# Optimization experiments

Measured on AMD Instinct MI355X. Metric: run time of the kernel, lower is better.

Reference implementation:

```python
import jax, jax.numpy as jnp
import numpy as np

B, T, C = 2, 2048, 1024
H = 16
D = C // H  # head size 64


def setup_inputs() -> dict:
    key = jax.random.key(0)
    ks = jax.random.split(key, 9)
    s = 0.02
    return {
        "x": jax.random.normal(ks[0], (B, T, C), dtype=jnp.float32),
        "Wq": jax.random.normal(ks[1], (C, C), dtype=jnp.float32) * s,
        "bq": jnp.zeros((C,), dtype=jnp.float32),
        "Wk": jax.random.normal(ks[2], (C, C), dtype=jnp.float32) * s,
        "bk": jnp.zeros((C,), dtype=jnp.float32),
        "Wv": jax.random.normal(ks[3], (C, C), dtype=jnp.float32) * s,
        "bv": jnp.zeros((C,), dtype=jnp.float32),
        "Wo": jax.random.normal(ks[4], (C, C), dtype=jnp.float32) * s,
        "bo": jnp.zeros((C,), dtype=jnp.float32),
    }


def reference(x, Wq, bq, Wk, bk, Wv, bv, Wo, bo):
    b, t, c = x.shape
    scale = 1.0 / jnp.sqrt(jnp.asarray(D, dtype=x.dtype))
    # projections (torch Linear: x @ W.T + b), then split heads -> [B,H,T,D]
    def split_heads(y):
        return y.reshape(b, t, H, D).transpose(0, 2, 1, 3)
    q = split_heads(x @ Wq.T + bq)
    k = split_heads(x @ Wk.T + bk)
    v = split_heads(x @ Wv.T + bv)
    # scores [B,H,T,T], causal mask (triu above diagonal = -inf)
    attn = jnp.einsum("bhqd,bhkd->bhqk", q, k) * scale
    causal = jnp.tril(jnp.ones((t, t), dtype=bool))  # True = keep
    attn = jnp.where(causal[None, None], attn, -jnp.inf)
    attn = jax.nn.softmax(attn, axis=-1)
    # dropout p=0.0 -> identity
    y = jnp.einsum("bhqk,bhkd->bhqd", attn, v)
    y = y.transpose(0, 2, 1, 3).reshape(b, t, c)
    return y @ Wo.T + bo
```

## Files before the change

kernel.cpp:

```cpp
#include <hip/hip_runtime.h>
#include <hip/hip_bf16.h>
#include <stdint.h>
#include <stddef.h>


typedef __bf16 bf16;
typedef __attribute__((ext_vector_type(8))) __bf16 bf16x8;
typedef __attribute__((ext_vector_type(4))) __bf16 bf16x4;
typedef __attribute__((ext_vector_type(4))) float floatx4;

#define MFMA_16x16x32(A, B, C) __builtin_amdgcn_mfma_f32_16x16x32_bf16(A, B, C, 0, 0, 0)

static constexpr int T_SEQ = 2048;
static constexpr int CDIM  = 1024;

__device__ __forceinline__ void gl2lds16(const bf16* g, bf16* l) {
  __builtin_amdgcn_global_load_lds(
      (const __attribute__((address_space(1))) uint32_t*)g,
      (__attribute__((address_space(3))) uint32_t*)l, 16, 0, 0);
}

__global__ __launch_bounds__(256) void convert_kernel(
    const float* __restrict__ x, const float* __restrict__ Wq,
    const float* __restrict__ Wk, const float* __restrict__ Wv,
    const float* __restrict__ Wo,
    bf16* __restrict__ Xb, bf16* __restrict__ Wqkvb, bf16* __restrict__ Wob) {
  size_t i = ((size_t)blockIdx.x * 256 + threadIdx.x) * 4;
  const float* src;
  bf16* dst;
  size_t off;
  if (i < 4194304) {
    src = x; dst = Xb; off = i;
  } else {
    size_t r = i - 4194304;
    int wsel = (int)(r >> 20);
    off = r & 1048575;
    src = (wsel == 0) ? Wq : (wsel == 1) ? Wk : (wsel == 2) ? Wv : Wo;
    dst = (wsel < 3) ? (Wqkvb + ((size_t)wsel << 20)) : Wob;
  }
  float4 v = *(const float4*)(src + off);
  bf16x4 o;
  o[0] = (bf16)v.x; o[1] = (bf16)v.y; o[2] = (bf16)v.z; o[3] = (bf16)v.w;
  *(bf16x4*)(dst + off) = o;
}

__global__ __launch_bounds__(256) void gemm_qkv(
    const bf16* __restrict__ Xb, const bf16* __restrict__ Wqkvb,
    const float* __restrict__ bq, const float* __restrict__ bk,
    const float* __restrict__ bv,
    bf16* __restrict__ Qb, bf16* __restrict__ Kb, bf16* __restrict__ Vtb) {
  __shared__ __align__(16) bf16 smem[12288];
  bf16* As = smem;
  bf16* Bs = smem + 4096;
  bf16* Cs = smem;

  const int bM = blockIdx.x & 63;
  const int bN = blockIdx.x >> 6;
  const int tid = threadIdx.x;
  const int w = tid >> 6, l = tid & 63;
  const int wm = w & 1, wn = w >> 1;
  const int lr = l >> 3, cl = l & 7;
  const int fr = l & 15, q4 = l >> 4;
  const int fc = fr;

  floatx4 acc[2][4];
#pragma unroll
  for (int mi = 0; mi < 2; ++mi)
#pragma unroll
    for (int ni = 0; ni < 4; ++ni)
#pragma unroll
      for (int r = 0; r < 4; ++r) acc[mi][ni][r] = 0.0f;

  for (int k0 = 0; k0 < CDIM; k0 += 64) {
#pragma unroll
    for (int i = 0; i < 2; ++i) {
      int row = i * 32 + w * 8 + lr;
      int cg = cl ^ (row & 7);
      gl2lds16(Xb + (size_t)(bM * 64 + row) * CDIM + k0 + cg * 8,
               As + row * 64 + cl * 8);
    }
#pragma unroll
    for (int i = 0; i < 4; ++i) {
      int row = i * 32 + w * 8 + lr;
      int cg = cl ^ (row & 7);
      gl2lds16(Wqkvb + (size_t)(bN * 128 + row) * CDIM + k0 + cg * 8,
               Bs + row * 64 + cl * 8);
    }
    __syncthreads();
#pragma unroll
    for (int kk = 0; kk < 2; ++kk) {
      const int cgk = kk * 4 + q4;
      bf16x8 af[2], bfr[4];
#pragma unroll
      for (int mi = 0; mi < 2; ++mi) {
        int row = wm * 32 + mi * 16 + fr;
        af[mi] = *(const bf16x8*)(As + row * 64 + (cgk ^ (row & 7)) * 8);
      }
#pragma unroll
      for (int ni = 0; ni < 4; ++ni) {
        int row = wn * 64 + ni * 16 + fr;
        bfr[ni] = *(const bf16x8*)(Bs + row * 64 + (cgk ^ (row & 7)) * 8);
      }
#pragma unroll
      for (int mi = 0; mi < 2; ++mi)
#pragma unroll
        for (int ni = 0; ni < 4; ++ni)
          acc[mi][ni] = MFMA_16x16x32(af[mi], bfr[ni], acc[mi][ni]);
    }
    __syncthreads();
  }

  const int seg = bN >> 3;
  const float QSCALE = 0.125f * 1.44269504089f;
  const float* bp = (seg == 0) ? bq : (seg == 1) ? bk : bv;

#pragma unroll
  for (int ni = 0; ni < 4; ++ni) {
    int jl = wn * 64 + ni * 16 + fc;
    float bias = bp[(bN * 128 + jl) & 1023];
#pragma unroll
    for (int mi = 0; mi < 2; ++mi)
#pragma unroll
      for (int r = 0; r < 4; ++r) {
        int ttl = wm * 32 + mi * 16 + q4 * 4 + r;
        float val = acc[mi][ni][r] + bias;
        if (seg == 0) val *= QSCALE;
        int addr = (seg == 2) ? jl * 72 + ttl : ttl * 136 + jl;
        Cs[addr] = (bf16)val;
      }
  }
  __syncthreads();

  if (seg < 2) {
    bf16* basep = (seg == 0) ? Qb : Kb;
    const int chunk = tid & 15;
    const int rb = (tid >> 4) * 4;
#pragma unroll
    for (int u = 0; u < 4; ++u) {
      int maj = rb + u;
      bf16x8 vdat = *(const bf16x8*)(Cs + maj * 136 + chunk * 8);
      int n = bM * 64 + maj;
      int b = n >> 11, tt = n & 2047;
      int j = bN * 128 + chunk * 8;
      int h = (j >> 6) & 15, d = j & 63;
      *(bf16x8*)(basep + (((size_t)(b * 16 + h) * T_SEQ + tt) << 6) + d) = vdat;
    }
  } else {
    const int chunk = tid & 7;
    const int rb = (tid >> 3) * 4;
#pragma unroll
    for (int u = 0; u < 4; ++u) {
      int maj = rb + u;
      bf16x8 vdat = *(const bf16x8*)(Cs + maj * 72 + chunk * 8);
      int j = bN * 128 + maj;
      int h = (j >> 6) & 15, d = j & 63;
      int n0 = bM * 64 + chunk * 8;
      int b = n0 >> 11, tt0 = n0 & 2047;
      *(bf16x8*)(Vtb + ((size_t)(b * 16 + h) * 64 + d) * T_SEQ + tt0) = vdat;
    }
  }
}

__global__ __launch_bounds__(256, 4) void flash_attn(
    const bf16* __restrict__ Qb, const bf16* __restrict__ Kb,
    const bf16* __restrict__ Vtb, bf16* __restrict__ Ao) {
  __shared__ __align__(16) bf16 Ks[64 * 64];
  __shared__ __align__(16) bf16 Ps[4][16 * 72];

  const int bh = blockIdx.x;
  const int ymap = blockIdx.y;
  const int a = ymap & 7, kq = ymap >> 3;
  const int qt = (kq == 0) ? 31 - a : (kq == 1) ? 16 + a : (kq == 2) ? 15 - a : a;
  const int b = bh >> 4, h = bh & 15;
  const int tid = threadIdx.x;
  const int w = tid >> 6, l = tid & 63;
  const int fc = l & 15, q4 = l >> 4;
  const int lr = l >> 3, cl = l & 7;

  const bf16* Qg = Qb + (size_t)bh * T_SEQ * 64;
  const bf16* Kg = Kb + (size_t)bh * T_SEQ * 64;
  const bf16* Vg = Vtb + (size_t)bh * 64 * T_SEQ;

  const int qrow = qt * 64 + w * 16 + fc;
  bf16x8 qf[2];
  qf[0] = *(const bf16x8*)(Qg + (size_t)qrow * 64 + q4 * 8);
  qf[1] = *(const bf16x8*)(Qg + (size_t)qrow * 64 + 32 + q4 * 8);

  const bf16* Vl = Vg + (size_t)fc * T_SEQ + q4 * 8;

  bf16x8 ones;
#pragma unroll
  for (int i = 0; i < 8; ++i) ones[i] = (bf16)1.0f;

  floatx4 o[4];
  floatx4 lacc;
#pragma unroll
  for (int ds = 0; ds < 4; ++ds)
#pragma unroll
    for (int r = 0; r < 4; ++r) o[ds][r] = 0.0f;
#pragma unroll
  for (int r = 0; r < 4; ++r) lacc[r] = 0.0f;

  for (int kv = 0; kv <= qt; ++kv) {
    const size_t kvb = (size_t)kv * 64;
#pragma unroll
    for (int i = 0; i < 2; ++i) {
      int row = i * 32 + w * 8 + lr;
      int cg = cl ^ (row & 7);
      gl2lds16(Kg + (kvb + row) * 64 + cg * 8, Ks + row * 64 + cl * 8);
    }
    __syncthreads();

    bf16x8 vf[2][4];
#pragma unroll
    for (int kk = 0; kk < 2; ++kk)
#pragma unroll
      for (int ds = 0; ds < 4; ++ds)
        vf[kk][ds] = *(const bf16x8*)(Vl + (size_t)(ds * 16) * T_SEQ + kvb + kk * 32);

    floatx4 s[4];
#pragma unroll
    for (int ni = 0; ni < 4; ++ni)
#pragma unroll
      for (int r = 0; r < 4; ++r) s[ni][r] = 0.0f;
#pragma unroll
    for (int kk = 0; kk < 2; ++kk) {
      const int cgk = kk * 4 + q4;
#pragma unroll
      for (int ni = 0; ni < 4; ++ni) {
        int row = ni * 16 + fc;
        bf16x8 kf = *(const bf16x8*)(Ks + row * 64 + (cgk ^ (row & 7)) * 8);
        s[ni] = MFMA_16x16x32(qf[kk], kf, s[ni]);
      }
    }

    if (kv == qt) {
      int qc = w * 16 + q4 * 4;
#pragma unroll
      for (int ni = 0; ni < 4; ++ni)
#pragma unroll
        for (int r = 0; r < 4; ++r) {
          int kc = ni * 16 + fc;
          float pv = (kc > qc + r) ? 0.0f : __builtin_amdgcn_exp2f(s[ni][r]);
          Ps[w][(q4 * 4 + r) * 72 + ni * 16 + fc] = (bf16)pv;
        }
    } else {
#pragma unroll
      for (int ni = 0; ni < 4; ++ni)
#pragma unroll
        for (int r = 0; r < 4; ++r)
          Ps[w][(q4 * 4 + r) * 72 + ni * 16 + fc] =
              (bf16)__builtin_amdgcn_exp2f(s[ni][r]);
    }

#pragma unroll
    for (int kk = 0; kk < 2; ++kk) {
      bf16x8 pf = *(const bf16x8*)(&Ps[w][fc * 72 + kk * 32 + q4 * 8]);
#pragma unroll
      for (int ds = 0; ds < 4; ++ds)
        o[ds] = MFMA_16x16x32(pf, vf[kk][ds], o[ds]);
      lacc = MFMA_16x16x32(pf, ones, lacc);
    }
    __syncthreads();
  }

  float inv[4];
#pragma unroll
  for (int r = 0; r < 4; ++r) inv[r] = __builtin_amdgcn_rcpf(lacc[r]);
#pragma unroll
  for (int ds = 0; ds < 4; ++ds)
#pragma unroll
    for (int r = 0; r < 4; ++r) {
      int tt = qt * 64 + w * 16 + q4 * 4 + r;
      int col = h * 64 + ds * 16 + fc;
      Ao[((size_t)(b * T_SEQ + tt) << 10) + col] = (bf16)(o[ds][r] * inv[r]);
    }
}

__global__ __launch_bounds__(256) void gemm_out(
    const bf16* __restrict__ Ab, const bf16* __restrict__ Wob,
    const float* __restrict__ bo, float* __restrict__ Y) {
  __shared__ __align__(16) bf16 As[64 * 64];
  __shared__ __align__(16) bf16 Bs[64 * 64];
  const int bM = blockIdx.x & 63;
  const int bN = blockIdx.x >> 6;
  const int tid = threadIdx.x;
  const int w = tid >> 6, l = tid & 63;
  const int wm = w & 1, wn = w >> 1;
  const int lr = l >> 3, cl = l & 7;
  const int fr = l & 15, q4 = l >> 4;
  const int fc = fr;

  floatx4 acc[2][2];
#pragma unroll
  for (int mi = 0; mi < 2; ++mi)
#pragma unroll
    for (int ni = 0; ni < 2; ++ni)
#pragma unroll
      for (int r = 0; r < 4; ++r) acc[mi][ni][r] = 0.0f;

  for (int k0 = 0; k0 < CDIM; k0 += 64) {
#pragma unroll
    for (int i = 0; i < 2; ++i) {
      int row = i * 32 + w * 8 + lr;
      int cg = cl ^ (row & 7);
      gl2lds16(Ab + (size_t)(bM * 64 + row) * CDIM + k0 + cg * 8,
               As + row * 64 + cl * 8);
      gl2lds16(Wob + (size_t)(bN * 64 + row) * CDIM + k0 + cg * 8,
               Bs + row * 64 + cl * 8);
    }
    __syncthreads();
#pragma unroll
    for (int kk = 0; kk < 2; ++kk) {
      const int cgk = kk * 4 + q4;
      bf16x8 af[2], bfr[2];
#pragma unroll
      for (int mi = 0; mi < 2; ++mi) {
        int row = wm * 32 + mi * 16 + fr;
        af[mi] = *(const bf16x8*)(As + row * 64 + (cgk ^ (row & 7)) * 8);
      }
#pragma unroll
      for (int ni = 0; ni < 2; ++ni) {
        int row = wn * 32 + ni * 16 + fr;
        bfr[ni] = *(const bf16x8*)(Bs + row * 64 + (cgk ^ (row & 7)) * 8);
      }
#pragma unroll
      for (int mi = 0; mi < 2; ++mi)
#pragma unroll
        for (int ni = 0; ni < 2; ++ni)
          acc[mi][ni] = MFMA_16x16x32(af[mi], bfr[ni], acc[mi][ni]);
    }
    __syncthreads();
  }

#pragma unroll
  for (int ni = 0; ni < 2; ++ni) {
    int j = bN * 64 + wn * 32 + ni * 16 + fc;
    float bias = bo[j];
#pragma unroll
    for (int mi = 0; mi < 2; ++mi)
#pragma unroll
      for (int r = 0; r < 4; ++r) {
        int n = bM * 64 + wm * 32 + mi * 16 + q4 * 4 + r;
        Y[(size_t)n * CDIM + j] = acc[mi][ni][r] + bias;
      }
  }
}

extern "C" void kernel_launch(void* const* d_in, const int* in_sizes, int n_in,
                              void* d_out, int out_size, void* d_ws, size_t ws_size,
                              hipStream_t stream) {
  const float* x  = (const float*)d_in[0];
  const float* Wq = (const float*)d_in[1];
  const float* bq = (const float*)d_in[2];
  const float* Wk = (const float*)d_in[3];
  const float* bk = (const float*)d_in[4];
  const float* Wv = (const float*)d_in[5];
  const float* bv = (const float*)d_in[6];
  const float* Wo = (const float*)d_in[7];
  const float* bo = (const float*)d_in[8];
  float* Y = (float*)d_out;

  char* ws = (char*)d_ws;
  const size_t MB = 1024 * 1024;
  bf16* Xb    = (bf16*)(ws + 0);
  bf16* Wqkvb = (bf16*)(ws + 8 * MB);
  bf16* Wob   = (bf16*)(ws + 14 * MB);
  bf16* Qb    = (bf16*)(ws + 16 * MB);
  bf16* Kb    = (bf16*)(ws + 24 * MB);
  bf16* Vtb   = (bf16*)(ws + 32 * MB);
  bf16* Ao    = Xb;

  convert_kernel<<<8192, 256, 0, stream>>>(x, Wq, Wk, Wv, Wo, Xb, Wqkvb, Wob);
  gemm_qkv<<<64 * 24, 256, 0, stream>>>(Xb, Wqkvb, bq, bk, bv, Qb, Kb, Vtb);
  flash_attn<<<dim3(32, 32), 256, 0, stream>>>(Qb, Kb, Vtb, Ao);
  gemm_out<<<64 * 16, 256, 0, stream>>>(Ao, Wob, bo, Y);
}
```

Before: 210.5 us.

## Split attention tile 2x2 across waves with LDS-staged V and final reduction

Restructures the flash attention block so each wave handles 32 query rows by 32 keys instead of 16 rows by 64 keys. Each K fragment is reused across two query subtiles, and V is now staged in swizzled LDS through global_load_lds instead of per-lane global loads. On the diagonal tile, waves whose key half lies fully above their query half skip all work. Partial O and row-sum accumulators from the two key-half waves are summed through LDS at the end, which adds an extra reduction pass and more shared memory per block.

```diff
diff --git a/kernel.cpp b/kernel.cpp
--- a/kernel.cpp
+++ b/kernel.cpp
@@ -164,8 +164,9 @@
 __global__ __launch_bounds__(256, 4) void flash_attn(
     const bf16* __restrict__ Qb, const bf16* __restrict__ Kb,
     const bf16* __restrict__ Vtb, bf16* __restrict__ Ao) {
-  __shared__ __align__(16) bf16 Ks[64 * 64];
-  __shared__ __align__(16) bf16 Ps[4][16 * 72];
+  __shared__ __align__(16) bf16 smem[15360];
+  bf16* Ks = smem;
+  bf16* Vs = smem + 4096;
 
   const int bh = blockIdx.x;
   const int ymap = blockIdx.y;
@@ -174,32 +175,39 @@
   const int b = bh >> 4, h = bh & 15;
   const int tid = threadIdx.x;
   const int w = tid >> 6, l = tid & 63;
+  const int wq = w & 1, ws = w >> 1;
   const int fc = l & 15, q4 = l >> 4;
   const int lr = l >> 3, cl = l & 7;
+  bf16* PsW = smem + 8192 + w * 1792;
 
   const bf16* Qg = Qb + (size_t)bh * T_SEQ * 64;
   const bf16* Kg = Kb + (size_t)bh * T_SEQ * 64;
   const bf16* Vg = Vtb + (size_t)bh * 64 * T_SEQ;
 
-  const int qrow = qt * 64 + w * 16 + fc;
-  bf16x8 qf[2];
-  qf[0] = *(const bf16x8*)(Qg + (size_t)qrow * 64 + q4 * 8);
-  qf[1] = *(const bf16x8*)(Qg + (size_t)qrow * 64 + 32 + q4 * 8);
-
-  const bf16* Vl = Vg + (size_t)fc * T_SEQ + q4 * 8;
+  bf16x8 qf[2][2];
+#pragma unroll
+  for (int mi = 0; mi < 2; ++mi) {
+    const bf16* qrow = Qg + (size_t)(qt * 64 + wq * 32 + mi * 16 + fc) * 64;
+#pragma unroll
+    for (int kk = 0; kk < 2; ++kk)
+      qf[mi][kk] = *(const bf16x8*)(qrow + kk * 32 + q4 * 8);
+  }
 
   bf16x8 ones;
 #pragma unroll
   for (int i = 0; i < 8; ++i) ones[i] = (bf16)1.0f;
 
-  floatx4 o[4];
-  floatx4 lacc;
-#pragma unroll
-  for (int ds = 0; ds < 4; ++ds)
-#pragma unroll
-    for (int r = 0; r < 4; ++r) o[ds][r] = 0.0f;
-#pragma unroll
-  for (int r = 0; r < 4; ++r) lacc[r] = 0.0f;
+  floatx4 o[2][4];
+  floatx4 lacc[2];
+#pragma unroll
+  for (int mi = 0; mi < 2; ++mi) {
+#pragma unroll
+    for (int ds = 0; ds < 4; ++ds)
+#pragma unroll
+      for (int r = 0; r < 4; ++r) o[mi][ds][r] = 0.0f;
+#pragma unroll
+    for (int r = 0; r < 4; ++r) lacc[mi][r] = 0.0f;
+  }
 
   for (int kv = 0; kv <= qt; ++kv) {
     const size_t kvb = (size_t)kv * 64;
@@ -208,73 +216,116 @@
       int row = i * 32 + w * 8 + lr;
       int cg = cl ^ (row & 7);
       gl2lds16(Kg + (kvb + row) * 64 + cg * 8, Ks + row * 64 + cl * 8);
-    }
-    __syncthreads();
-
-    bf16x8 vf[2][4];
-#pragma unroll
-    for (int kk = 0; kk < 2; ++kk)
+      gl2lds16(Vg + (size_t)row * T_SEQ + kvb + cg * 8, Vs + row * 64 + cl * 8);
+    }
+    __syncthreads();
+
+    const bool diag = (kv == qt);
+    const bool skipall = diag && (ws > wq);
+
+    if (!skipall) {
+      floatx4 s[2][2];
+#pragma unroll
+      for (int mi = 0; mi < 2; ++mi)
+#pragma unroll
+        for (int ni = 0; ni < 2; ++ni)
+#pragma unroll
+          for (int r = 0; r < 4; ++r) s[mi][ni][r] = 0.0f;
+#pragma unroll
+      for (int kk = 0; kk < 2; ++kk) {
+        const int cgk = kk * 4 + q4;
+#pragma unroll
+        for (int ni = 0; ni < 2; ++ni) {
+          int row = ws * 32 + ni * 16 + fc;
+          bf16x8 kf = *(const bf16x8*)(Ks + row * 64 + (cgk ^ (row & 7)) * 8);
+          s[0][ni] = MFMA_16x16x32(qf[0][kk], kf, s[0][ni]);
+          s[1][ni] = MFMA_16x16x32(qf[1][kk], kf, s[1][ni]);
+        }
+      }
+
+      if (diag && (ws == wq)) {
+#pragma unroll
+        for (int mi = 0; mi < 2; ++mi)
+#pragma unroll
+          for (int ni = 0; ni < 2; ++ni)
+#pragma unroll
+            for (int r = 0; r < 4; ++r) {
+              int kc = ni * 16 + fc, qc = mi * 16 + q4 * 4 + r;
+              float pv = (kc > qc) ? 0.0f : __builtin_amdgcn_exp2f(s[mi][ni][r]);
+              PsW[(mi * 16 + q4 * 4 + r) * 56 + ni * 16 + fc] = (bf16)pv;
+            }
+      } else {
+#pragma unroll
+        for (int mi = 0; mi < 2; ++mi)
+#pragma unroll
+          for (int ni = 0; ni < 2; ++ni)
+#pragma unroll
+            for (int r = 0; r < 4; ++r)
+              PsW[(mi * 16 + q4 * 4 + r) * 56 + ni * 16 + fc] =
+                  (bf16)__builtin_amdgcn_exp2f(s[mi][ni][r]);
+      }
+
+      bf16x8 pf[2];
+#pragma unroll
+      for (int mi = 0; mi < 2; ++mi)
+        pf[mi] = *(const bf16x8*)(&PsW[(mi * 16 + fc) * 56 + q4 * 8]);
+      const int cgv = ws * 4 + q4;
+#pragma unroll
+      for (int ds = 0; ds < 4; ++ds) {
+        int row = ds * 16 + fc;
+        bf16x8 vf = *(const bf16x8*)(Vs + row * 64 + (cgv ^ (row & 7)) * 8);
+        o[0][ds] = MFMA_16x16x32(pf[0], vf, o[0][ds]);
+        o[1][ds] = MFMA_16x16x32(pf[1], vf, o[1][ds]);
+      }
+      lacc[0] = MFMA_16x16x32(pf[0], ones, lacc[0]);
+      lacc[1] = MFMA_16x16x32(pf[1], ones, lacc[1]);
+    }
+    __syncthreads();
+  }
+
+  __syncthreads();
+  float* red = (float*)smem;
+  const int rbase = wq * 2560 + l * 4;
+  if (ws == 1) {
+#pragma unroll
+    for (int mi = 0; mi < 2; ++mi)
 #pragma unroll
       for (int ds = 0; ds < 4; ++ds)
-        vf[kk][ds] = *(const bf16x8*)(Vl + (size_t)(ds * 16) * T_SEQ + kvb + kk * 32);
-
-    floatx4 s[4];
-#pragma unroll
-    for (int ni = 0; ni < 4; ++ni)
-#pragma unroll
-      for (int r = 0; r < 4; ++r) s[ni][r] = 0.0f;
-#pragma unroll
-    for (int kk = 0; kk < 2; ++kk) {
-      const int cgk = kk * 4 + q4;
-#pragma unroll
-      for (int ni = 0; ni < 4; ++ni) {
-        int row = ni * 16 + fc;
-        bf16x8 kf = *(const bf16x8*)(Ks + row * 64 + (cgk ^ (row & 7)) * 8);
-        s[ni] = MFMA_16x16x32(qf[kk], kf, s[ni]);
-      }
-    }
-
-    if (kv == qt) {
-      int qc = w * 16 + q4 * 4;
-#pragma unroll
-      for (int ni = 0; ni < 4; ++ni)
+        *(floatx4*)(red + rbase + (mi * 4 + ds) * 256) = o[mi][ds];
+    *(floatx4*)(red + rbase + 8 * 256) = lacc[0];
+    *(floatx4*)(red + rbase + 9 * 256) = lacc[1];
+  }
+  __syncthreads();
+  if (ws == 0) {
+#pragma unroll
+    for (int mi = 0; mi < 2; ++mi)
+#pragma unroll
+      for (int ds = 0; ds < 4; ++ds) {
+        floatx4 t = *(const floatx4*)(red + rbase + (mi * 4 + ds) * 256);
+#pragma unroll
+        for (int r = 0; r < 4; ++r) o[mi][ds][r] += t[r];
+      }
+    floatx4 t0 = *(const floatx4*)(red + rbase + 8 * 256);
+    floatx4 t1 = *(const floatx4*)(red + rbase + 9 * 256);
+#pragma unroll
+    for (int r = 0; r < 4; ++r) { lacc[0][r] += t0[r]; lacc[1][r] += t1[r]; }
+
+#pragma unroll
+    for (int mi = 0; mi < 2; ++mi) {
+      float inv[4];
+#pragma unroll
+      for (int r = 0; r < 4; ++r) inv[r] = __builtin_amdgcn_rcpf(lacc[mi][r]);
+#pragma unroll
+      for (int ds = 0; ds < 4; ++ds)
 #pragma unroll
         for (int r = 0; r < 4; ++r) {
-          int kc = ni * 16 + fc;
-          float pv = (kc > qc + r) ? 0.0f : __builtin_amdgcn_exp2f(s[ni][r]);
-          Ps[w][(q4 * 4 + r) * 72 + ni * 16 + fc] = (bf16)pv;
+          int tt = qt * 64 + wq * 32 + mi * 16 + q4 * 4 + r;
+          int col = h * 64 + ds * 16 + fc;
+          Ao[((size_t)(b * T_SEQ + tt) << 10) + col] =
+              (bf16)(o[mi][ds][r] * inv[r]);
         }
-    } else {
-#pragma unroll
-      for (int ni = 0; ni < 4; ++ni)
-#pragma unroll
-        for (int r = 0; r < 4; ++r)
-          Ps[w][(q4 * 4 + r) * 72 + ni * 16 + fc] =
-              (bf16)__builtin_amdgcn_exp2f(s[ni][r]);
-    }
-
-#pragma unroll
-    for (int kk = 0; kk < 2; ++kk) {
-      bf16x8 pf = *(const bf16x8*)(&Ps[w][fc * 72 + kk * 32 + q4 * 8]);
-#pragma unroll
-      for (int ds = 0; ds < 4; ++ds)
-        o[ds] = MFMA_16x16x32(pf, vf[kk][ds], o[ds]);
-      lacc = MFMA_16x16x32(pf, ones, lacc);
-    }
-    __syncthreads();
-  }
-
-  float inv[4];
-#pragma unroll
-  for (int r = 0; r < 4; ++r) inv[r] = __builtin_amdgcn_rcpf(lacc[r]);
-#pragma unroll
-  for (int ds = 0; ds < 4; ++ds)
-#pragma unroll
-    for (int r = 0; r < 4; ++r) {
-      int tt = qt * 64 + w * 16 + q4 * 4 + r;
-      int col = h * 64 + ds * 16 + fc;
-      Ao[((size_t)(b * T_SEQ + tt) << 10) + col] = (bf16)(o[ds][r] * inv[r]);
-    }
+    }
+  }
 }
 
 __global__ __launch_bounds__(256) void gemm_out(
```

Measured after the change: 176.0 us. -16.4%, faster.
